# Kernel tuning notes

Hardware: AMD Instinct MI355X
Metric: run time of the kernel (lower is better)

Reference implementation:

```python
import jax, jax.numpy as jnp
import numpy as np

B, N, C, H = 16, 1024, 768, 12
HD = C // H               # head_dim = 64
SCALE = HD ** -0.5
EPS = 1e-5


def ter_quant(w):
    """BitNet-b1.58 ternary weight quantization with straight-through estimator.
    Per-tensor scale = mean(|W|); weights rounded to {-1,0,1}*scale."""
    s = jnp.mean(jnp.abs(w))
    wq = jnp.round(jnp.clip(w / (s + EPS), -1.0, 1.0)) * s
    return w + jax.lax.stop_gradient(wq - w)


def setup_inputs() -> dict:
    key = jax.random.key(0)
    k1, k2, k3 = jax.random.split(key, 3)
    return {
        "x": jax.random.normal(k1, (B, N, C), dtype=jnp.float32),
        "w_qkv": jax.random.normal(k2, (3 * C, C), dtype=jnp.float32) * 0.02,
        "w_proj": jax.random.normal(k3, (C, C), dtype=jnp.float32) * 0.02,
        "b_proj": jnp.zeros((C,), dtype=jnp.float32),
    }


def reference(x, w_qkv, w_proj, b_proj):
    # ternary-quantized QKV projection: [B,N,C] @ [C,3C] -> [B,N,3C]
    qkv = jnp.einsum('bnc,dc->bnd', x, ter_quant(w_qkv))
    qkv = qkv.reshape(B, N, 3, H, HD).transpose(2, 0, 3, 1, 4)  # [3,B,H,N,HD]
    q, k, v = qkv[0], qkv[1], qkv[2]
    # manual softmax attention (dropout p=0 -> identity)
    attn = jax.nn.softmax(jnp.einsum('bhqd,bhkd->bhqk', q, k) * SCALE, axis=-1)
    out = jnp.einsum('bhqk,bhkd->bhqd', attn, v)          # [B,H,N,HD]
    out = out.transpose(0, 2, 1, 3).reshape(B, N, C)      # [B,N,C]
    # ternary-quantized output projection
    return jnp.einsum('bnc,dc->bnd', out, ter_quant(w_proj)) + b_proj
```

## Files before the change

kernel.cpp:

```cpp
#include <hip/hip_runtime.h>
#include <hip/hip_bf16.h>

#define DEVI __device__ __forceinline__

typedef __bf16 bf16_t;
typedef __bf16 bf16x8 __attribute__((ext_vector_type(8)));
typedef float  f32x4  __attribute__((ext_vector_type(4)));
typedef float  f32x16 __attribute__((ext_vector_type(16)));
typedef unsigned short u16x4 __attribute__((ext_vector_type(4)));
typedef unsigned int   u32x4 __attribute__((ext_vector_type(4)));

typedef __attribute__((address_space(1))) unsigned int gas_u32;
typedef __attribute__((address_space(3))) unsigned int las_u32;

#define LOG2E 1.4426950408889634f

DEVI void gload16(const void* g, void* l) {
  __builtin_amdgcn_global_load_lds((gas_u32*)g, (las_u32*)l, 16, 0, 0);
}

DEVI unsigned short bf16bits(float f) {
  bf16_t b = (bf16_t)f;
  return __builtin_bit_cast(unsigned short, b);
}

DEVI unsigned pk2(float a, float b) {
  return ((unsigned)bf16bits(b) << 16) | (unsigned)bf16bits(a);
}

DEVI unsigned short quant1(float wv, double s) {
  double tq = (double)wv / s;
  tq = fmin(fmax(tq, -1.0), 1.0);
  return __builtin_bit_cast(unsigned short, (bf16_t)(float)rint(tq));
}

__global__ __launch_bounds__(256) void k_abssum2(const float* __restrict__ wq,
                                                 const float* __restrict__ wp,
                                                 double* __restrict__ partials) {
  __shared__ double sm[256];
  const int t = threadIdx.x, bid = blockIdx.x;
  const float* __restrict__ w = (bid < 256) ? wq : wp;
  const int n = (bid < 256) ? 1769472 : 589824;
  const int b0 = bid & 255;
  double acc = 0.0;
  for (int i = b0 * 256 + t; i < n; i += 65536)
    acc += (double)fabsf(w[i]);
  sm[t] = acc;
  __syncthreads();
  #pragma unroll
  for (int s = 128; s > 0; s >>= 1) {
    if (t < s) sm[t] += sm[t + s];
    __syncthreads();
  }
  if (t == 0) partials[bid] = sm[0];
}

__global__ __launch_bounds__(256) void k_reduce2(const double* __restrict__ partials,
                                                 double* __restrict__ outs) {
  __shared__ double sm[256];
  const int t = threadIdx.x;
  sm[t] = partials[blockIdx.x * 256 + t];
  __syncthreads();
  #pragma unroll
  for (int s = 128; s > 0; s >>= 1) {
    if (t < s) sm[t] += sm[t + s];
    __syncthreads();
  }
  if (t == 0) outs[blockIdx.x] = sm[0];
}

__global__ __launch_bounds__(256) void k_prep(
    const float* __restrict__ wq, const float* __restrict__ wp,
    const float* __restrict__ x, const double* __restrict__ scl,
    bf16_t* __restrict__ wqs, bf16_t* __restrict__ wps, bf16_t* __restrict__ xbf) {
  const int bid = blockIdx.x, t = threadIdx.x;
  if (bid < 1728) {
    const double s = scl[0] * (1.0 / 1769472.0) + 1e-5;
    const int i = bid * 256 + t;
    const float4 v = ((const float4*)wq)[i];
    u16x4 o = { quant1(v.x, s), quant1(v.y, s), quant1(v.z, s), quant1(v.w, s) };
    ((u16x4*)wqs)[i] = o;
  } else if (bid < 2304) {
    const double s = scl[1] * (1.0 / 589824.0) + 1e-5;
    const int i = (bid - 1728) * 256 + t;
    const float4 v = ((const float4*)wp)[i];
    u16x4 o = { quant1(v.x, s), quant1(v.y, s), quant1(v.z, s), quant1(v.w, s) };
    ((u16x4*)wps)[i] = o;
  } else {
    const int i = (bid - 2304) * 256 + t;
    const float4 v = ((const float4*)x)[i];
    u16x4 pk = { bf16bits(v.x), bf16bits(v.y), bf16bits(v.z), bf16bits(v.w) };
    ((u16x4*)xbf)[i] = pk;
  }
}

template<int MODE>
__global__ __launch_bounds__(512, 4) void k_gemm(
    const bf16_t* __restrict__ A, const bf16_t* __restrict__ Bw,
    const double* __restrict__ sumptr, double invn,
    bf16_t* __restrict__ Qb, bf16_t* __restrict__ Kb, bf16_t* __restrict__ VTb,
    const float* __restrict__ bias, float* __restrict__ Out,
    int nxblk)
{
  __shared__ __align__(16) char lds[73728];
  const int t = threadIdx.x, l = t & 63, w = t >> 6;

  const int nblk = nxblk * 64;
  const int flat = blockIdx.y * nxblk + blockIdx.x;
  const int per = nblk >> 3;
  const int swz = (flat & 7) * per + (flat >> 3);
  const int m0 = (swz / nxblk) * 256, n0 = (swz % nxblk) * 128;

  const int wm = w >> 1, wn = w & 1;
  const int lq = l & 15, lh = l >> 4;
  const int grow = t >> 2, gs8 = (t & 3) * 8;

  auto stage = [&](int slot, int kts) {
    char* dst = lds + slot * 24576;
    gload16(A + (size_t)(m0 + grow) * 768 + kts * 32 + gs8, dst + t * 16);
    gload16(A + (size_t)(m0 + 128 + grow) * 768 + kts * 32 + gs8, dst + 8192 + t * 16);
    gload16(Bw + (size_t)(n0 + grow) * 768 + kts * 32 + gs8, dst + 16384 + t * 16);
  };

  f32x4 acc[4][4] = {};

  stage(0, 0);
  stage(1, 1);
  asm volatile("s_waitcnt vmcnt(3)" ::: "memory");
  asm volatile("s_barrier" ::: "memory");

  #pragma unroll
  for (int kt = 0; kt < 24; ++kt) {
    const char* cA = lds + (kt % 3) * 24576 + (wm >> 1) * 8192;
    const char* cB = lds + (kt % 3) * 24576 + 16384;

    bf16x8 af[4], bf[4];
    #pragma unroll
    for (int i = 0; i < 4; ++i) {
      const int lrow = (wm & 1) * 64 + i * 16 + lq;
      af[i] = *(const bf16x8*)(cA + lrow * 64 + lh * 16);
    }
    #pragma unroll
    for (int j = 0; j < 4; ++j) {
      const int row = wn * 64 + j * 16 + lq;
      bf[j] = *(const bf16x8*)(cB + row * 64 + lh * 16);
    }
    if (kt < 22) stage((kt + 2) % 3, kt + 2);
    __builtin_amdgcn_s_setprio(1);
    #pragma unroll
    for (int i = 0; i < 4; ++i)
      #pragma unroll
      for (int j = 0; j < 4; ++j)
        acc[i][j] = __builtin_amdgcn_mfma_f32_16x16x32_bf16(af[i], bf[j], acc[i][j], 0, 0, 0);
    __builtin_amdgcn_s_setprio(0);
    if (kt <= 21)      asm volatile("s_waitcnt vmcnt(3)" ::: "memory");
    else if (kt == 22) asm volatile("s_waitcnt vmcnt(0)" ::: "memory");
    asm volatile("s_barrier" ::: "memory");
  }

  const float s = (float)((*sumptr) * invn);
  char* st = lds + w * 8192;

  const int mrow0 = m0 + wm * 64;
  const int b = mrow0 >> 10, nbase = mrow0 & 1023;

  if (MODE == 0) {
    const int d0 = n0 + wn * 64;
    const int which = d0 / 768;
    const int hh = (d0 >> 6) % 12;
    if (which == 2) {
      #pragma unroll
      for (int j = 0; j < 4; ++j)
        #pragma unroll
        for (int i = 0; i < 4; ++i)
          #pragma unroll
          for (int r = 0; r < 4; ++r) {
            const int rowd = j * 16 + lq;
            const int coln = (i * 16 + lh * 4 + r) * 2;
            *(bf16_t*)(st + rowd * 128 + (coln ^ ((rowd & 7) << 4))) =
                (bf16_t)(acc[i][j][r] * s);
          }
    } else {
      const float sc = (which == 0) ? s * 0.125f * LOG2E : s;
      #pragma unroll
      for (int i = 0; i < 4; ++i)
        #pragma unroll
        for (int j = 0; j < 4; ++j)
          #pragma unroll
          for (int r = 0; r < 4; ++r) {
            const int row = i * 16 + lh * 4 + r;
            const int colb = (j * 16 + lq) * 2;
            *(bf16_t*)(st + row * 128 + (colb ^ ((row & 7) << 4))) =
                (bf16_t)(acc[i][j][r] * sc);
          }
    }
    __syncthreads();
    if (which == 0) {
      char* dstp = (char*)(Qb + ((size_t)(b * 12 + hh) * 1024 + nbase) * 64);
      #pragma unroll
      for (int it = 0; it < 8; ++it) {
        const int row = it * 8 + (l >> 3);
        const int colb = (l & 7) * 16;
        const u32x4 v = *(const u32x4*)(st + row * 128 + (colb ^ ((row & 7) << 4)));
        *(u32x4*)(dstp + row * 128 + colb) = v;
      }
    } else {
      bf16_t* base = (which == 1) ? Kb : VTb;
      char* dstp = (char*)base + ((((size_t)(b * 12 + hh)) * 16 + (nbase >> 6)) << 13);
      #pragma unroll
      for (int j = 0; j < 8; ++j) {
        const int row = (j >> 2) * 32 + (l & 31);
        const int colb = (j & 3) * 32 + (l >> 5) * 16;
        const u32x4 v = *(const u32x4*)(st + row * 128 + (colb ^ ((row & 7) << 4)));
        *(u32x4*)(dstp + j * 1024 + l * 16) = v;
      }
    }
  } else {
    const int d0 = n0 + wn * 64;
    const float4 bv = *(const float4*)(bias + d0 + (l & 15) * 4);
    #pragma unroll
    for (int c = 0; c < 2; ++c) {
      #pragma unroll
      for (int i2 = 0; i2 < 2; ++i2) {
        const int i = c * 2 + i2;
        #pragma unroll
        for (int j = 0; j < 4; ++j)
          #pragma unroll
          for (int r = 0; r < 4; ++r) {
            const int row = i2 * 16 + lh * 4 + r;
            const int colb = (j * 16 + lq) * 4;
            *(float*)(st + row * 256 + (colb ^ ((row & 7) << 4))) = acc[i][j][r] * s;
          }
      }
      __syncthreads();
      #pragma unroll
      for (int it = 0; it < 8; ++it) {
        const int row = it * 4 + (l >> 4);
        const int colb = (l & 15) * 16;
        float4 v = *(const float4*)(st + row * 256 + (colb ^ ((row & 7) << 4)));
        v.x += bv.x; v.y += bv.y; v.z += bv.z; v.w += bv.w;
        *(float4*)((char*)(Out + (size_t)(mrow0 + c * 32 + row) * 768 + d0) + colb) = v;
      }
      __syncthreads();
    }
  }
}

__global__ __launch_bounds__(256, 4) void k_attn(
    const bf16_t* __restrict__ Qb, const bf16_t* __restrict__ Kb,
    const bf16_t* __restrict__ VTb, bf16_t* __restrict__ Ob)
{
  __shared__ bf16_t smem[2][2][4096];
  const int t = threadIdx.x, l = t & 63, w = t >> 6;
  const int bh = blockIdx.x, qb = blockIdx.y;
  const int lq = l & 31, hi = l >> 5;
  const int q0 = qb * 128 + w * 32;

  const char* Kg = (const char*)(Kb + (size_t)bh * 65536);
  const char* Vg = (const char*)(VTb + (size_t)bh * 65536);

  bf16x8 qf[4];
  #pragma unroll
  for (int ks = 0; ks < 4; ++ks)
    qf[ks] = *(const bf16x8*)(Qb + (size_t)bh * 65536 + (q0 + lq) * 64 + ks * 16 + hi * 8);

  const u32x4 onesw = {0x3F803F80u, 0x3F803F80u, 0x3F803F80u, 0x3F803F80u};
  const bf16x8 onesf = __builtin_bit_cast(bf16x8, onesw);

  f32x16 ot0 = {}, ot1 = {}, ps = {};

  auto stage = [&](int buf, int kt) {
    #pragma unroll
    for (int i = 0; i < 2; ++i) {
      const int c = i * 4 + w;
      gload16(Kg + (size_t)kt * 8192 + c * 1024 + l * 16, &smem[buf][0][c * 512]);
      gload16(Vg + (size_t)kt * 8192 + c * 1024 + l * 16, &smem[buf][1][c * 512]);
    }
  };

  stage(0, 0);
  __syncthreads();

  for (int kt = 0; kt < 16; ++kt) {
    const int cur = kt & 1;
    if (kt < 15) stage(cur ^ 1, kt + 1);
    const char* lK = (const char*)smem[cur][0];
    const char* lV = (const char*)smem[cur][1];
    const int lo = l * 16;

    f32x16 st0 = {}, st1 = {};
    __builtin_amdgcn_s_setprio(1);
    #pragma unroll
    for (int ks = 0; ks < 4; ++ks) {
      const bf16x8 k0 = *(const bf16x8*)(lK + ks * 1024 + lo);
      const bf16x8 k1 = *(const bf16x8*)(lK + (4 + ks) * 1024 + lo);
      st0 = __builtin_amdgcn_mfma_f32_32x32x16_bf16(k0, qf[ks], st0, 0, 0, 0);
      st1 = __builtin_amdgcn_mfma_f32_32x32x16_bf16(k1, qf[ks], st1, 0, 0, 0);
    }
    __builtin_amdgcn_s_setprio(0);

    __builtin_amdgcn_s_setprio(1);
    auto grp = [&](const f32x16& stv, int r0, int g) {
      float p[8];
      #pragma unroll
      for (int e = 0; e < 8; ++e) p[e] = __builtin_amdgcn_exp2f(stv[r0 + e]);
      const unsigned w0 = pk2(p[0], p[1]), w1 = pk2(p[2], p[3]);
      const unsigned w2 = pk2(p[4], p[5]), w3 = pk2(p[6], p[7]);
      const unsigned x0 = __shfl_xor(w0, 32), x1 = __shfl_xor(w1, 32);
      const unsigned x2 = __shfl_xor(w2, 32), x3 = __shfl_xor(w3, 32);
      const u32x4 fw = hi ? u32x4{x2, x3, w2, w3} : u32x4{w0, w1, x0, x1};
      const bf16x8 pf = __builtin_bit_cast(bf16x8, fw);
      const bf16x8 v0 = *(const bf16x8*)(lV + g * 1024 + lo);
      const bf16x8 v1 = *(const bf16x8*)(lV + (4 + g) * 1024 + lo);
      ot0 = __builtin_amdgcn_mfma_f32_32x32x16_bf16(v0, pf, ot0, 0, 0, 0);
      ot1 = __builtin_amdgcn_mfma_f32_32x32x16_bf16(v1, pf, ot1, 0, 0, 0);
      ps  = __builtin_amdgcn_mfma_f32_32x32x16_bf16(onesf, pf, ps, 0, 0, 0);
    };
    grp(st0, 0, 0);
    grp(st0, 8, 1);
    grp(st1, 0, 2);
    grp(st1, 8, 3);
    __builtin_amdgcn_s_setprio(0);

    __syncthreads();
  }

  __syncthreads();
  bf16_t* olds = (bf16_t*)smem + w * 2048;
  const float inv = 1.0f / ps[0];
  #pragma unroll
  for (int dt = 0; dt < 2; ++dt)
    #pragma unroll
    for (int rg = 0; rg < 4; ++rg) {
      u16x4 pk;
      #pragma unroll
      for (int e = 0; e < 4; ++e)
        pk[e] = bf16bits((dt ? ot1[rg * 4 + e] : ot0[rg * 4 + e]) * inv);
      const int d = rg * 8 + hi * 4 + dt * 32;
      *(u16x4*)((char*)olds + ((lq * 128 + d * 2) ^ ((lq & 7) << 4))) = pk;
    }
  __syncthreads();
  const int b = bh / 12, h = bh % 12;
  #pragma unroll
  for (int i = 0; i < 8; ++i) {
    const int q = i * 4 + (l >> 4);
    const u16x4 v =
        *(const u16x4*)((const char*)olds + ((q * 128 + (l & 15) * 8) ^ ((q & 7) << 4)));
    *(u16x4*)(Ob + ((size_t)(b * 1024 + q0 + q)) * 768 + h * 64 + (l & 15) * 4) = v;
  }
}

extern "C" void kernel_launch(void* const* d_in, const int* in_sizes, int n_in,
                              void* d_out, int out_size, void* d_ws, size_t ws_size,
                              hipStream_t stream) {
  const float* x      = (const float*)d_in[0];
  const float* w_qkv  = (const float*)d_in[1];
  const float* w_proj = (const float*)d_in[2];
  const float* b_proj = (const float*)d_in[3];
  float* out = (float*)d_out;

  char* ws = (char*)d_ws;
  double* part  = (double*)ws;
  double* scl   = (double*)(ws + 4096);
  bf16_t* xbf   = (bf16_t*)(ws + 4608);
  bf16_t* wqs   = (bf16_t*)(ws + 4608 + 25165824);
  bf16_t* wps   = (bf16_t*)(ws + 4608 + 25165824 + 3538944);
  bf16_t* qbuf  = (bf16_t*)(ws + 4608 + 25165824 + 3538944 + 1179648);
  bf16_t* kbuf  = qbuf + 12582912;
  bf16_t* vtbuf = kbuf + 12582912;
  bf16_t* aout  = xbf;

  k_abssum2<<<512, 256, 0, stream>>>(w_qkv, w_proj, part);
  k_reduce2<<<2, 256, 0, stream>>>(part, scl);
  k_prep<<<14592, 256, 0, stream>>>(w_qkv, w_proj, x, scl, wqs, wps, xbf);
  k_gemm<0><<<dim3(18, 64), 512, 0, stream>>>(xbf, wqs, scl, 1.0 / 1769472.0,
                                              qbuf, kbuf, vtbuf, nullptr, nullptr, 18);
  k_attn<<<dim3(192, 8), 256, 0, stream>>>(qbuf, kbuf, vtbuf, aout);
  k_gemm<1><<<dim3(6, 64), 512, 0, stream>>>(aout, wps, scl + 1, 1.0 / 589824.0,
                                             nullptr, nullptr, nullptr, b_proj, out, 6);
}
```

Baseline: 189.5 us.

## Process two query tiles per wave in attention and sum row totals in VALU

Each attention wave now handles 64 query rows as two 32-row tiles, so every K and V fragment read from LDS feeds twice as many MFMAs, and the grid's query-block dimension is halved. The row-sum MFMA against a ones vector is replaced by scalar adds of the exponentials plus a cross-half shuffle, which removes one third of the PV-stage MFMAs. This raises register pressure, so launch bounds drop to two blocks per SIMD-group, which may lower occupancy and latency hiding. The row sum is now taken from fp32 values instead of the bf16-rounded ones.

After: 188.2 us. No clear change (-0.7%).

```diff
diff --git a/kernel.cpp b/kernel.cpp
--- a/kernel.cpp
+++ b/kernel.cpp
@@ -246,7 +246,7 @@
   }
 }
 
-__global__ __launch_bounds__(256, 4) void k_attn(
+__global__ __launch_bounds__(256, 2) void k_attn(
     const bf16_t* __restrict__ Qb, const bf16_t* __restrict__ Kb,
     const bf16_t* __restrict__ VTb, bf16_t* __restrict__ Ob)
 {
@@ -254,20 +254,20 @@
   const int t = threadIdx.x, l = t & 63, w = t >> 6;
   const int bh = blockIdx.x, qb = blockIdx.y;
   const int lq = l & 31, hi = l >> 5;
-  const int q0 = qb * 128 + w * 32;
+  const int q0 = qb * 256 + w * 64;
 
   const char* Kg = (const char*)(Kb + (size_t)bh * 65536);
   const char* Vg = (const char*)(VTb + (size_t)bh * 65536);
 
-  bf16x8 qf[4];
-  #pragma unroll
-  for (int ks = 0; ks < 4; ++ks)
-    qf[ks] = *(const bf16x8*)(Qb + (size_t)bh * 65536 + (q0 + lq) * 64 + ks * 16 + hi * 8);
-
-  const u32x4 onesw = {0x3F803F80u, 0x3F803F80u, 0x3F803F80u, 0x3F803F80u};
-  const bf16x8 onesf = __builtin_bit_cast(bf16x8, onesw);
-
-  f32x16 ot0 = {}, ot1 = {}, ps = {};
+  bf16x8 qfA[4], qfB[4];
+  #pragma unroll
+  for (int ks = 0; ks < 4; ++ks) {
+    qfA[ks] = *(const bf16x8*)(Qb + (size_t)bh * 65536 + (q0 + lq) * 64 + ks * 16 + hi * 8);
+    qfB[ks] = *(const bf16x8*)(Qb + (size_t)bh * 65536 + (q0 + 32 + lq) * 64 + ks * 16 + hi * 8);
+  }
+
+  f32x16 oA0 = {}, oA1 = {}, oB0 = {}, oB1 = {};
+  float lA = 0.0f, lB = 0.0f;
 
   auto stage = [&](int buf, int kt) {
     #pragma unroll
@@ -288,64 +288,89 @@
     const char* lV = (const char*)smem[cur][1];
     const int lo = l * 16;
 
-    f32x16 st0 = {}, st1 = {};
+    f32x16 sA0 = {}, sA1 = {}, sB0 = {}, sB1 = {};
     __builtin_amdgcn_s_setprio(1);
     #pragma unroll
     for (int ks = 0; ks < 4; ++ks) {
       const bf16x8 k0 = *(const bf16x8*)(lK + ks * 1024 + lo);
       const bf16x8 k1 = *(const bf16x8*)(lK + (4 + ks) * 1024 + lo);
-      st0 = __builtin_amdgcn_mfma_f32_32x32x16_bf16(k0, qf[ks], st0, 0, 0, 0);
-      st1 = __builtin_amdgcn_mfma_f32_32x32x16_bf16(k1, qf[ks], st1, 0, 0, 0);
+      sA0 = __builtin_amdgcn_mfma_f32_32x32x16_bf16(k0, qfA[ks], sA0, 0, 0, 0);
+      sA1 = __builtin_amdgcn_mfma_f32_32x32x16_bf16(k1, qfA[ks], sA1, 0, 0, 0);
+      sB0 = __builtin_amdgcn_mfma_f32_32x32x16_bf16(k0, qfB[ks], sB0, 0, 0, 0);
+      sB1 = __builtin_amdgcn_mfma_f32_32x32x16_bf16(k1, qfB[ks], sB1, 0, 0, 0);
     }
     __builtin_amdgcn_s_setprio(0);
 
+    float psA = 0.0f, psB = 0.0f;
     __builtin_amdgcn_s_setprio(1);
-    auto grp = [&](const f32x16& stv, int r0, int g) {
-      float p[8];
-      #pragma unroll
-      for (int e = 0; e < 8; ++e) p[e] = __builtin_amdgcn_exp2f(stv[r0 + e]);
-      const unsigned w0 = pk2(p[0], p[1]), w1 = pk2(p[2], p[3]);
-      const unsigned w2 = pk2(p[4], p[5]), w3 = pk2(p[6], p[7]);
-      const unsigned x0 = __shfl_xor(w0, 32), x1 = __shfl_xor(w1, 32);
-      const unsigned x2 = __shfl_xor(w2, 32), x3 = __shfl_xor(w3, 32);
-      const u32x4 fw = hi ? u32x4{x2, x3, w2, w3} : u32x4{w0, w1, x0, x1};
-      const bf16x8 pf = __builtin_bit_cast(bf16x8, fw);
+    auto grpAB = [&](const f32x16& svA, const f32x16& svB, int r0, int g) {
+      float pA[8], pB[8];
+      #pragma unroll
+      for (int e = 0; e < 8; ++e) pA[e] = __builtin_amdgcn_exp2f(svA[r0 + e]);
+      #pragma unroll
+      for (int e = 0; e < 8; ++e) pB[e] = __builtin_amdgcn_exp2f(svB[r0 + e]);
+      psA += ((pA[0] + pA[1]) + (pA[2] + pA[3])) + ((pA[4] + pA[5]) + (pA[6] + pA[7]));
+      psB += ((pB[0] + pB[1]) + (pB[2] + pB[3])) + ((pB[4] + pB[5]) + (pB[6] + pB[7]));
+      const unsigned a0 = pk2(pA[0], pA[1]), a1 = pk2(pA[2], pA[3]);
+      const unsigned a2 = pk2(pA[4], pA[5]), a3 = pk2(pA[6], pA[7]);
+      const unsigned b0 = pk2(pB[0], pB[1]), b1 = pk2(pB[2], pB[3]);
+      const unsigned b2 = pk2(pB[4], pB[5]), b3 = pk2(pB[6], pB[7]);
+      const unsigned xa0 = __shfl_xor(a0, 32), xa1 = __shfl_xor(a1, 32);
+      const unsigned xa2 = __shfl_xor(a2, 32), xa3 = __shfl_xor(a3, 32);
+      const unsigned xb0 = __shfl_xor(b0, 32), xb1 = __shfl_xor(b1, 32);
+      const unsigned xb2 = __shfl_xor(b2, 32), xb3 = __shfl_xor(b3, 32);
+      const u32x4 fwA = hi ? u32x4{xa2, xa3, a2, a3} : u32x4{a0, a1, xa0, xa1};
+      const u32x4 fwB = hi ? u32x4{xb2, xb3, b2, b3} : u32x4{b0, b1, xb0, xb1};
+      const bf16x8 pfA = __builtin_bit_cast(bf16x8, fwA);
+      const bf16x8 pfB = __builtin_bit_cast(bf16x8, fwB);
       const bf16x8 v0 = *(const bf16x8*)(lV + g * 1024 + lo);
       const bf16x8 v1 = *(const bf16x8*)(lV + (4 + g) * 1024 + lo);
-      ot0 = __builtin_amdgcn_mfma_f32_32x32x16_bf16(v0, pf, ot0, 0, 0, 0);
-      ot1 = __builtin_amdgcn_mfma_f32_32x32x16_bf16(v1, pf, ot1, 0, 0, 0);
-      ps  = __builtin_amdgcn_mfma_f32_32x32x16_bf16(onesf, pf, ps, 0, 0, 0);
+      oA0 = __builtin_amdgcn_mfma_f32_32x32x16_bf16(v0, pfA, oA0, 0, 0, 0);
+      oA1 = __builtin_amdgcn_mfma_f32_32x32x16_bf16(v1, pfA, oA1, 0, 0, 0);
+      oB0 = __builtin_amdgcn_mfma_f32_32x32x16_bf16(v0, pfB, oB0, 0, 0, 0);
+      oB1 = __builtin_amdgcn_mfma_f32_32x32x16_bf16(v1, pfB, oB1, 0, 0, 0);
     };
-    grp(st0, 0, 0);
-    grp(st0, 8, 1);
-    grp(st1, 0, 2);
-    grp(st1, 8, 3);
+    grpAB(sA0, sB0, 0, 0);
+    grpAB(sA0, sB0, 8, 1);
+    grpAB(sA1, sB1, 0, 2);
+    grpAB(sA1, sB1, 8, 3);
     __builtin_amdgcn_s_setprio(0);
+    psA += __shfl_xor(psA, 32);
+    psB += __shfl_xor(psB, 32);
+    lA += psA;
+    lB += psB;
 
     __syncthreads();
   }
 
   __syncthreads();
-  bf16_t* olds = (bf16_t*)smem + w * 2048;
-  const float inv = 1.0f / ps[0];
-  #pragma unroll
-  for (int dt = 0; dt < 2; ++dt)
-    #pragma unroll
-    for (int rg = 0; rg < 4; ++rg) {
-      u16x4 pk;
-      #pragma unroll
-      for (int e = 0; e < 4; ++e)
-        pk[e] = bf16bits((dt ? ot1[rg * 4 + e] : ot0[rg * 4 + e]) * inv);
-      const int d = rg * 8 + hi * 4 + dt * 32;
-      *(u16x4*)((char*)olds + ((lq * 128 + d * 2) ^ ((lq & 7) << 4))) = pk;
-    }
+  char* olds = (char*)smem + w * 8192;
+  const float invA = 1.0f / lA, invB = 1.0f / lB;
+  #pragma unroll
+  for (int half = 0; half < 2; ++half) {
+    const float inv = half ? invB : invA;
+    #pragma unroll
+    for (int dt = 0; dt < 2; ++dt)
+      #pragma unroll
+      for (int rg = 0; rg < 4; ++rg) {
+        u16x4 pk;
+        #pragma unroll
+        for (int e = 0; e < 4; ++e) {
+          const float val = half ? (dt ? oB1[rg * 4 + e] : oB0[rg * 4 + e])
+                                 : (dt ? oA1[rg * 4 + e] : oA0[rg * 4 + e]);
+          pk[e] = bf16bits(val * inv);
+        }
+        const int d = rg * 8 + hi * 4 + dt * 32;
+        *(u16x4*)(olds + half * 4096 + ((lq * 128 + d * 2) ^ ((lq & 7) << 4))) = pk;
+      }
+  }
   __syncthreads();
   const int b = bh / 12, h = bh % 12;
   #pragma unroll
-  for (int i = 0; i < 8; ++i) {
+  for (int i = 0; i < 16; ++i) {
     const int q = i * 4 + (l >> 4);
     const u16x4 v =
-        *(const u16x4*)((const char*)olds + ((q * 128 + (l & 15) * 8) ^ ((q & 7) << 4)));
+        *(const u16x4*)(olds + ((q * 128 + (l & 15) * 8) ^ ((q & 7) << 4)));
     *(u16x4*)(Ob + ((size_t)(b * 1024 + q0 + q)) * 768 + h * 64 + (l & 15) * 4) = v;
   }
 }
@@ -375,7 +400,7 @@
   k_prep<<<14592, 256, 0, stream>>>(w_qkv, w_proj, x, scl, wqs, wps, xbf);
   k_gemm<0><<<dim3(18, 64), 512, 0, stream>>>(xbf, wqs, scl, 1.0 / 1769472.0,
                                               qbuf, kbuf, vtbuf, nullptr, nullptr, 18);
-  k_attn<<<dim3(192, 8), 256, 0, stream>>>(qbuf, kbuf, vtbuf, aout);
+  k_attn<<<dim3(192, 4), 256, 0, stream>>>(qbuf, kbuf, vtbuf, aout);
   k_gemm<1><<<dim3(6, 64), 512, 0, stream>>>(aout, wps, scl + 1, 1.0 / 589824.0,
                                              nullptr, nullptr, nullptr, b_proj, out, 6);
 }
```
